# Kernel tuning notes

Hardware: AMD Instinct MI355X
Metric: run time of the kernel (lower is better)

Reference implementation:

```python
import jax, jax.numpy as jnp
import numpy as np

B, T = 64, 16            # batch, action horizon
ACTION_DIM = 32
HIDDEN = 1536            # config.input_embedding_dim
NUM_CAT = 4              # config.max_num_embodiments
NUM_BUCKETS = 1000       # config.num_timestep_buckets


def setup_inputs() -> dict:
    key = jax.random.key(0)
    ks = jax.random.split(key, 6)
    return {
        "actions": jax.random.normal(ks[0], (B, T, ACTION_DIM), jnp.float32),
        "timesteps": jax.random.randint(ks[1], (B,), 0, NUM_BUCKETS, dtype=jnp.int32),
        "cat_ids": jax.random.randint(ks[2], (B,), 0, NUM_CAT, dtype=jnp.int32),
        # CategorySpecificLinear params: W ~ 0.02*randn, b = zeros (as in torch init)
        "W1": 0.02 * jax.random.normal(ks[3], (NUM_CAT, ACTION_DIM, HIDDEN), jnp.float32),
        "b1": jnp.zeros((NUM_CAT, HIDDEN), jnp.float32),
        "W2": 0.02 * jax.random.normal(ks[4], (NUM_CAT, 2 * HIDDEN, HIDDEN), jnp.float32),
        "b2": jnp.zeros((NUM_CAT, HIDDEN), jnp.float32),
        "W3": 0.02 * jax.random.normal(ks[5], (NUM_CAT, HIDDEN, HIDDEN), jnp.float32),
        "b3": jnp.zeros((NUM_CAT, HIDDEN), jnp.float32),
    }


def cs_linear(x, W, b, onehot):
    """CategorySpecificLinear: equivalent to bmm(x, W[cat_ids]) + b[cat_ids].
    Grouped form avoids materializing the (B, Din, Dout) gathered weight tensor:
    compute per-category results (C=4 is tiny) and select via one-hot.
    x: (B,T,Din)  W: (C,Din,Dout)  b: (C,Dout)  onehot: (B,C)
    """
    y = jnp.einsum('btd,cdh->bcth', x, W)        # (B,C,T,Dout)
    y = jnp.einsum('bcth,bc->bth', y, onehot)    # select own category
    return y + (onehot @ b)[:, None, :]


def sinusoidal_pe(t, dim):
    """Standard sinusoidal positional encoding of scalar positions t (B,T) -> (B,T,dim)."""
    half = dim // 2
    freqs = jnp.exp(-np.log(10000.0) * jnp.arange(half, dtype=jnp.float32) / half)
    ang = t.astype(jnp.float32)[..., None] * freqs  # (B,T,half)
    return jnp.concatenate([jnp.sin(ang), jnp.cos(ang)], axis=-1)


def reference(actions, timesteps, cat_ids, W1, b1, W2, b2, W3, b3):
    onehot = jax.nn.one_hot(cat_ids, W1.shape[0], dtype=actions.dtype)  # (B,C)
    t = jnp.broadcast_to(timesteps[:, None], actions.shape[:2])          # (B,T)
    a_emb = cs_linear(actions, W1, b1, onehot)                            # (B,T,H)
    tau_emb = sinusoidal_pe(t, a_emb.shape[-1]).astype(a_emb.dtype)       # (B,T,H)
    x = jnp.concatenate([a_emb, tau_emb], axis=-1)                        # (B,T,2H)
    h = cs_linear(x, W2, b2, onehot)
    h = h * jax.nn.sigmoid(h)                                             # swish
    return cs_linear(h, W3, b3, onehot)                                   # (B,T,H)
```

## Files before the change

### kernel.cpp

```cpp
#include <hip/hip_runtime.h>
#include <hip/hip_bf16.h>

#define BB 64
#define TT 16
#define ROWS 1024
#define ADIM 32
#define HID 1536
#define NCAT 4
#define MT_MAX 20

typedef __attribute__((ext_vector_type(8))) short bf16x8;
typedef __attribute__((ext_vector_type(4))) float f32x4;

static __device__ __forceinline__ unsigned short f2bf(float f) {
    union { float f; unsigned int u; } v; v.f = f;
    unsigned int u = v.u + 0x7fff + ((v.u >> 16) & 1);
    return (unsigned short)(u >> 16);
}

__global__ void prep_kernel(const int* __restrict__ cat_ids,
                            int* __restrict__ msample, int* __restrict__ mcat) {
    __shared__ int counts[NCAT];
    const int t = threadIdx.x;
    if (t < NCAT) {
        int c = 0;
        for (int s = 0; s < BB; ++s) c += (cat_ids[s] == t);
        counts[t] = c;
    }
    __syncthreads();
    if (t < NCAT) {
        int off = 0;
        for (int c = 0; c < t; ++c) off += (counts[c] + 3) >> 2;
        const int mt = (counts[t] + 3) >> 2;
        int idx = 0;
        for (int s = 0; s < BB; ++s)
            if (cat_ids[s] == t) msample[off * 4 + (idx++)] = s;
        for (; idx < mt * 4; ++idx) msample[off * 4 + idx] = -1;
        for (int m = 0; m < mt; ++m) mcat[off + m] = t;
    }
    __syncthreads();
    if (t == 0) {
        int tot = 0;
        for (int c = 0; c < NCAT; ++c) tot += (counts[c] + 3) >> 2;
        for (int m = tot; m < MT_MAX; ++m) mcat[m] = -1;
    }
}

__global__ void build_x_kernel(const float* __restrict__ actions,
                               const int* __restrict__ timesteps,
                               const int* __restrict__ cat_ids,
                               const float* __restrict__ W1,
                               const float* __restrict__ b1,
                               unsigned short* __restrict__ X) {
    const int s = blockIdx.x;
    const int part = blockIdx.y;
    const int t = threadIdx.x;
    if (part < 6) {
        const int cat = cat_ids[s];
        const int h = part * 256 + t;
        __shared__ float act[TT][ADIM];
        const float* ab = actions + (size_t)s * TT * ADIM;
        ((float*)act)[t]       = ab[t];
        ((float*)act)[t + 256] = ab[t + 256];
        __syncthreads();
        const float* W1c = W1 + (size_t)cat * ADIM * HID + h;
        float acc[TT];
        #pragma unroll
        for (int r = 0; r < TT; ++r) acc[r] = 0.f;
        #pragma unroll 8
        for (int d = 0; d < ADIM; ++d) {
            const float w = W1c[(size_t)d * HID];
            #pragma unroll
            for (int r = 0; r < TT; ++r) acc[r] += act[r][d] * w;
        }
        const float bias = b1[cat * HID + h];
        #pragma unroll
        for (int r = 0; r < TT; ++r)
            X[(size_t)(s * TT + r) * (2 * HID) + h] = f2bf(acc[r] + bias);
    } else {
        const float ts = (float)timesteps[s];
        #pragma unroll
        for (int j = 0; j < 6; ++j) {
            const int i = j * 256 + t;
            const int ii = (i < 768) ? i : i - 768;
            const float freq = expf(-9.210340371976184f * (float)ii * (1.0f / 768.0f));
            const float ang = ts * freq;
            const float v = (i < 768) ? sinf(ang) : cosf(ang);
            const unsigned short bv = f2bf(v);
            for (int r = 0; r < TT; ++r)
                X[(size_t)(s * TT + r) * (2 * HID) + HID + i] = bv;
        }
    }
}

template<int K, int S>
__global__ __launch_bounds__(64) void gemm_part_kernel(
        const unsigned short* __restrict__ X,
        const float* __restrict__ W,
        const int* __restrict__ msample,
        const int* __restrict__ mcat,
        float* __restrict__ P) {
    const int m = blockIdx.y;
    const int cat = mcat[m];
    if (cat < 0) return;
    const int n0 = blockIdx.x * 64;
    const int ks = blockIdx.z;
    constexpr int KP = K / S;
    const int k0 = ks * KP;
    const int lane = threadIdx.x;
    const int col = lane & 15;
    const int g = lane >> 4;

    int sidx[4];
    #pragma unroll
    for (int f = 0; f < 4; ++f) sidx[f] = msample[m * 4 + f];

    const unsigned short* arow[4];
    #pragma unroll
    for (int f = 0; f < 4; ++f) {
        const int s = sidx[f] < 0 ? 0 : sidx[f];
        arow[f] = X + (size_t)(s * TT + col) * K + k0 + g * 8;
    }
    const float* wbase = W + ((size_t)cat * K + k0 + g * 8) * HID + n0 + col;

    f32x4 acc[4][4];
    #pragma unroll
    for (int f = 0; f < 4; ++f)
        #pragma unroll
        for (int c = 0; c < 4; ++c) acc[f][c] = f32x4{0.f, 0.f, 0.f, 0.f};

    for (int kk = 0; kk < KP; kk += 32) {
        bf16x8 a[4];
        #pragma unroll
        for (int f = 0; f < 4; ++f)
            a[f] = *(const bf16x8*)(arow[f] + kk);
        const float* wp = wbase + (size_t)kk * HID;
        #pragma unroll
        for (int c = 0; c < 4; ++c) {
            bf16x8 b;
            #pragma unroll
            for (int j = 0; j < 8; ++j) {
                const float w = wp[(size_t)j * HID + c * 16];
                b[j] = (short)f2bf(w);
            }
            #pragma unroll
            for (int f = 0; f < 4; ++f)
                acc[f][c] = __builtin_amdgcn_mfma_f32_16x16x32_bf16(a[f], b, acc[f][c], 0, 0, 0);
        }
    }

    #pragma unroll
    for (int f = 0; f < 4; ++f) {
        if (sidx[f] < 0) continue;
        #pragma unroll
        for (int c = 0; c < 4; ++c) {
            #pragma unroll
            for (int r = 0; r < 4; ++r) {
                const int row = sidx[f] * TT + g * 4 + r;
                P[((size_t)ks * ROWS + row) * HID + n0 + c * 16 + col] = acc[f][c][r];
            }
        }
    }
}

template<int S, bool DOSWISH, bool BF16OUT>
__global__ void finish_kernel(const float* __restrict__ P,
                              const float* __restrict__ bias,
                              const int* __restrict__ cat_ids,
                              void* __restrict__ out) {
    const int idx = blockIdx.x * 256 + threadIdx.x;
    const int i4 = idx * 4;
    const int row = i4 / HID;
    const int colb = i4 - row * HID;
    const int cat = cat_ids[row >> 4];
    float4 v = *(const float4*)(P + i4);
    #pragma unroll
    for (int s2 = 1; s2 < S; ++s2) {
        const float4 p = *(const float4*)(P + (size_t)s2 * ROWS * HID + i4);
        v.x += p.x; v.y += p.y; v.z += p.z; v.w += p.w;
    }
    const float4 bv = *(const float4*)(bias + (size_t)cat * HID + colb);
    v.x += bv.x; v.y += bv.y; v.z += bv.z; v.w += bv.w;
    if (DOSWISH) {
        v.x = v.x / (1.f + __expf(-v.x));
        v.y = v.y / (1.f + __expf(-v.y));
        v.z = v.z / (1.f + __expf(-v.z));
        v.w = v.w / (1.f + __expf(-v.w));
    }
    if (BF16OUT) {
        uint2 u;
        u.x = (unsigned)f2bf(v.x) | ((unsigned)f2bf(v.y) << 16);
        u.y = (unsigned)f2bf(v.z) | ((unsigned)f2bf(v.w) << 16);
        *(uint2*)((unsigned short*)out + i4) = u;
    } else {
        *(float4*)((float*)out + i4) = v;
    }
}

extern "C" void kernel_launch(void* const* d_in, const int* in_sizes, int n_in,
                              void* d_out, int out_size, void* d_ws, size_t ws_size,
                              hipStream_t stream) {
    const float* actions   = (const float*)d_in[0];
    const int*   timesteps = (const int*)d_in[1];
    const int*   cat_ids   = (const int*)d_in[2];
    const float* W1        = (const float*)d_in[3];
    const float* b1        = (const float*)d_in[4];
    const float* W2        = (const float*)d_in[5];
    const float* b2        = (const float*)d_in[6];
    const float* W3        = (const float*)d_in[7];
    const float* b3        = (const float*)d_in[8];

    char* ws = (char*)d_ws;
    unsigned short* X = (unsigned short*)ws;
    unsigned short* H = (unsigned short*)(ws + 6291456);
    float* P          = (float*)(ws + 9437184);
    int* msample      = (int*)(ws + 34603008);
    int* mcat         = msample + MT_MAX * 4;

    prep_kernel<<<1, 64, 0, stream>>>(cat_ids, msample, mcat);
    build_x_kernel<<<dim3(BB, 7), 256, 0, stream>>>(actions, timesteps, cat_ids, W1, b1, X);

    gemm_part_kernel<2 * HID, 4><<<dim3(HID / 64, MT_MAX, 4), 64, 0, stream>>>(
        X, W2, msample, mcat, P);
    finish_kernel<4, true, true><<<ROWS * HID / 4 / 256, 256, 0, stream>>>(
        P, b2, cat_ids, H);

    gemm_part_kernel<HID, 4><<<dim3(HID / 64, MT_MAX, 4), 64, 0, stream>>>(
        H, W3, msample, mcat, P);
    finish_kernel<4, false, false><<<ROWS * HID / 4 / 256, 256, 0, stream>>>(
        P, b3, cat_ids, d_out);
}
```

Baseline: 102.8 us.

## Rewrite grouped GEMM with LDS double-buffered 64x128 tiles and fewer K splits

After: 123.9 us. 20.4% more time.

```diff
diff --git a/kernel.cpp b/kernel.cpp
--- a/kernel.cpp
+++ b/kernel.cpp
@@ -1,5 +1,6 @@
 #include <hip/hip_runtime.h>
 #include <hip/hip_bf16.h>
+#include <stdint.h>
 
 #define BB 64
 #define TT 16
@@ -8,6 +9,8 @@
 #define HID 1536
 #define NCAT 4
 #define MT_MAX 20
+#define KP 768
+#define NTILES (KP/64)
 
 typedef __attribute__((ext_vector_type(8))) short bf16x8;
 typedef __attribute__((ext_vector_type(4))) float f32x4;
@@ -36,13 +39,13 @@
         for (int s = 0; s < BB; ++s)
             if (cat_ids[s] == t) msample[off * 4 + (idx++)] = s;
         for (; idx < mt * 4; ++idx) msample[off * 4 + idx] = -1;
-        for (int m = 0; m < mt; ++m) mcat[off + m] = t;
+        for (int mm = 0; mm < mt; ++mm) mcat[off + mm] = t;
     }
     __syncthreads();
     if (t == 0) {
         int tot = 0;
         for (int c = 0; c < NCAT; ++c) tot += (counts[c] + 3) >> 2;
-        for (int m = tot; m < MT_MAX; ++m) mcat[m] = -1;
+        for (int mm = tot; mm < MT_MAX; ++mm) mcat[mm] = -1;
     }
 }
 
@@ -69,9 +72,9 @@
         for (int r = 0; r < TT; ++r) acc[r] = 0.f;
         #pragma unroll 8
         for (int d = 0; d < ADIM; ++d) {
-            const float w = W1c[(size_t)d * HID];
-            #pragma unroll
-            for (int r = 0; r < TT; ++r) acc[r] += act[r][d] * w;
+            const float wv = W1c[(size_t)d * HID];
+            #pragma unroll
+            for (int r = 0; r < TT; ++r) acc[r] += act[r][d] * wv;
         }
         const float bias = b1[cat * HID + h];
         #pragma unroll
@@ -93,73 +96,135 @@
     }
 }
 
-template<int K, int S>
-__global__ __launch_bounds__(64) void gemm_part_kernel(
-        const unsigned short* __restrict__ X,
+template<int K>
+__global__ __launch_bounds__(256) void gemm_cs2(
+        const unsigned short* __restrict__ Xin,
         const float* __restrict__ W,
         const int* __restrict__ msample,
         const int* __restrict__ mcat,
         float* __restrict__ P) {
-    const int m = blockIdx.y;
+    const int m   = blockIdx.y;
     const int cat = mcat[m];
     if (cat < 0) return;
-    const int n0 = blockIdx.x * 64;
+    const int n0 = blockIdx.x * 128;
     const int ks = blockIdx.z;
-    constexpr int KP = K / S;
     const int k0 = ks * KP;
-    const int lane = threadIdx.x;
-    const int col = lane & 15;
-    const int g = lane >> 4;
-
-    int sidx[4];
+
+    const int q  = threadIdx.x;
+    const int l  = q & 63;
+    const int w  = q >> 6;
+    const int wm = w >> 1, wn = w & 1;
+    const int col = l & 15, g = l >> 4;
+
+    __shared__ unsigned short Abuf[2][8][64][8];
+    __shared__ unsigned short Bbuf[2][8][128][8];
+
+    const int s0 = msample[m*4+0], s1 = msample[m*4+1],
+              s2 = msample[m*4+2], s3 = msample[m*4+3];
+
+    int sA = (g == 0) ? s0 : (g == 1) ? s1 : (g == 2) ? s2 : s3;
+    if (sA < 0) sA = 0;
+    const unsigned short* aSrc = Xin + ((size_t)sA * TT + col) * K + k0;
+
+    const float* wbase = W + ((size_t)cat * K + k0) * HID + n0;
+
+    f32x4 acc[2][4];
     #pragma unroll
-    for (int f = 0; f < 4; ++f) sidx[f] = msample[m * 4 + f];
-
-    const unsigned short* arow[4];
+    for (int i = 0; i < 2; ++i)
+        #pragma unroll
+        for (int j = 0; j < 4; ++j) acc[i][j] = f32x4{0.f, 0.f, 0.f, 0.f};
+
+    float bcol[4][8];
+
+#if __has_builtin(__builtin_amdgcn_global_load_lds)
+    auto issueA = [&](int t, int buf) {
+        #pragma unroll
+        for (int pp = 0; pp < 2; ++pp) {
+            const int p = w * 2 + pp;
+            __builtin_amdgcn_global_load_lds(
+                (const __attribute__((address_space(1))) unsigned int*)(aSrc + t * 64 + p * 8),
+                (__attribute__((address_space(3))) unsigned int*)(&Abuf[buf][p][0][0]),
+                16, 0, 0);
+        }
+    };
+#else
+    const int rowF = q >> 2;
+    int sF = (w == 0) ? s0 : (w == 1) ? s1 : (w == 2) ? s2 : s3;
+    if (sF < 0) sF = 0;
+    const unsigned short* aSrcF = Xin + ((size_t)sF * TT + (rowF & 15)) * K + k0;
+    auto issueA = [&](int t, int buf) {
+        #pragma unroll
+        for (int it = 0; it < 2; ++it) {
+            const int slot = (q & 3) + it * 4;
+            bf16x8 av = *(const bf16x8*)(aSrcF + t * 64 + slot * 8);
+            *(bf16x8*)(&Abuf[buf][slot][rowF][0]) = av;
+        }
+    };
+#endif
+
+    auto loadB = [&](int t) {
+        #pragma unroll
+        for (int it = 0; it < 4; ++it) {
+            const int c = q + it * 256;
+            const int n = c & 127, slot = c >> 7;
+            const float* wc = wbase + ((size_t)t * 64 + slot * 8) * HID + n;
+            #pragma unroll
+            for (int dk = 0; dk < 8; ++dk) bcol[it][dk] = wc[(size_t)dk * HID];
+        }
+    };
+    auto cvtWriteB = [&](int buf) {
+        #pragma unroll
+        for (int it = 0; it < 4; ++it) {
+            const int c = q + it * 256;
+            const int n = c & 127, slot = c >> 7;
+            bf16x8 v;
+            #pragma unroll
+            for (int dk = 0; dk < 8; ++dk) v[dk] = (short)f2bf(bcol[it][dk]);
+            *(bf16x8*)(&Bbuf[buf][slot][n][0]) = v;
+        }
+    };
+    auto compute = [&](int buf) {
+        #pragma unroll
+        for (int kc = 0; kc < 2; ++kc) {
+            const int sl = kc * 4 + g;
+            const bf16x8 a0 = *(const bf16x8*)(&Abuf[buf][sl][wm * 32 + col][0]);
+            const bf16x8 a1 = *(const bf16x8*)(&Abuf[buf][sl][wm * 32 + 16 + col][0]);
+            #pragma unroll
+            for (int nf = 0; nf < 4; ++nf) {
+                const bf16x8 bb = *(const bf16x8*)(&Bbuf[buf][sl][wn * 64 + nf * 16 + col][0]);
+                acc[0][nf] = __builtin_amdgcn_mfma_f32_16x16x32_bf16(a0, bb, acc[0][nf], 0, 0, 0);
+                acc[1][nf] = __builtin_amdgcn_mfma_f32_16x16x32_bf16(a1, bb, acc[1][nf], 0, 0, 0);
+            }
+        }
+    };
+
+    issueA(0, 0);
+    loadB(0);
+    cvtWriteB(0);
+    __syncthreads();
+    for (int t = 0; t < NTILES - 1; ++t) {
+        const int cur = t & 1, nxt = cur ^ 1;
+        loadB(t + 1);
+        issueA(t + 1, nxt);
+        compute(cur);
+        cvtWriteB(nxt);
+        __syncthreads();
+    }
+    compute((NTILES - 1) & 1);
+
+    const int sE0 = wm ? s2 : s0;
+    const int sE1 = wm ? s3 : s1;
     #pragma unroll
-    for (int f = 0; f < 4; ++f) {
-        const int s = sidx[f] < 0 ? 0 : sidx[f];
-        arow[f] = X + (size_t)(s * TT + col) * K + k0 + g * 8;
-    }
-    const float* wbase = W + ((size_t)cat * K + k0 + g * 8) * HID + n0 + col;
-
-    f32x4 acc[4][4];
-    #pragma unroll
-    for (int f = 0; f < 4; ++f)
-        #pragma unroll
-        for (int c = 0; c < 4; ++c) acc[f][c] = f32x4{0.f, 0.f, 0.f, 0.f};
-
-    for (int kk = 0; kk < KP; kk += 32) {
-        bf16x8 a[4];
-        #pragma unroll
-        for (int f = 0; f < 4; ++f)
-            a[f] = *(const bf16x8*)(arow[f] + kk);
-        const float* wp = wbase + (size_t)kk * HID;
-        #pragma unroll
-        for (int c = 0; c < 4; ++c) {
-            bf16x8 b;
-            #pragma unroll
-            for (int j = 0; j < 8; ++j) {
-                const float w = wp[(size_t)j * HID + c * 16];
-                b[j] = (short)f2bf(w);
-            }
-            #pragma unroll
-            for (int f = 0; f < 4; ++f)
-                acc[f][c] = __builtin_amdgcn_mfma_f32_16x16x32_bf16(a[f], b, acc[f][c], 0, 0, 0);
-        }
-    }
-
-    #pragma unroll
-    for (int f = 0; f < 4; ++f) {
-        if (sidx[f] < 0) continue;
-        #pragma unroll
-        for (int c = 0; c < 4; ++c) {
-            #pragma unroll
-            for (int r = 0; r < 4; ++r) {
-                const int row = sidx[f] * TT + g * 4 + r;
-                P[((size_t)ks * ROWS + row) * HID + n0 + c * 16 + col] = acc[f][c][r];
-            }
-        }
+    for (int mf = 0; mf < 2; ++mf) {
+        const int s = mf ? sE1 : sE0;
+        if (s < 0) continue;
+        float* prow = P + ((size_t)ks * ROWS + (size_t)s * TT + g * 4) * HID
+                        + n0 + wn * 64 + col;
+        #pragma unroll
+        for (int nf = 0; nf < 4; ++nf)
+            #pragma unroll
+            for (int j = 0; j < 4; ++j)
+                prow[(size_t)j * HID + nf * 16] = acc[mf][nf][j];
     }
 }
 
@@ -220,13 +285,13 @@
     prep_kernel<<<1, 64, 0, stream>>>(cat_ids, msample, mcat);
     build_x_kernel<<<dim3(BB, 7), 256, 0, stream>>>(actions, timesteps, cat_ids, W1, b1, X);
 
-    gemm_part_kernel<2 * HID, 4><<<dim3(HID / 64, MT_MAX, 4), 64, 0, stream>>>(
+    gemm_cs2<2 * HID><<<dim3(HID / 128, MT_MAX, 4), 256, 0, stream>>>(
         X, W2, msample, mcat, P);
     finish_kernel<4, true, true><<<ROWS * HID / 4 / 256, 256, 0, stream>>>(
         P, b2, cat_ids, H);
 
-    gemm_part_kernel<HID, 4><<<dim3(HID / 64, MT_MAX, 4), 64, 0, stream>>>(
+    gemm_cs2<HID><<<dim3(HID / 128, MT_MAX, 2), 256, 0, stream>>>(
         H, W3, msample, mcat, P);
-    finish_kernel<4, false, false><<<ROWS * HID / 4 / 256, 256, 0, stream>>>(
+    finish_kernel<2, false, false><<<ROWS * HID / 4 / 256, 256, 0, stream>>>(
         P, b3, cat_ids, d_out);
 }
```

## Software-pipeline GEMM loads with triple-buffered registers and reduce W3 split-K

Applied to the files above, without the earlier changes.

Measured after the change: 119.6 us. +16.3%, slower.

```diff
diff --git a/kernel.cpp b/kernel.cpp
--- a/kernel.cpp
+++ b/kernel.cpp
@@ -36,13 +36,13 @@
         for (int s = 0; s < BB; ++s)
             if (cat_ids[s] == t) msample[off * 4 + (idx++)] = s;
         for (; idx < mt * 4; ++idx) msample[off * 4 + idx] = -1;
-        for (int m = 0; m < mt; ++m) mcat[off + m] = t;
+        for (int mm = 0; mm < mt; ++mm) mcat[off + mm] = t;
     }
     __syncthreads();
     if (t == 0) {
         int tot = 0;
         for (int c = 0; c < NCAT; ++c) tot += (counts[c] + 3) >> 2;
-        for (int m = tot; m < MT_MAX; ++m) mcat[m] = -1;
+        for (int mm = tot; mm < MT_MAX; ++mm) mcat[mm] = -1;
     }
 }
 
@@ -69,9 +69,9 @@
         for (int r = 0; r < TT; ++r) acc[r] = 0.f;
         #pragma unroll 8
         for (int d = 0; d < ADIM; ++d) {
-            const float w = W1c[(size_t)d * HID];
-            #pragma unroll
-            for (int r = 0; r < TT; ++r) acc[r] += act[r][d] * w;
+            const float wv = W1c[(size_t)d * HID];
+            #pragma unroll
+            for (int r = 0; r < TT; ++r) acc[r] += act[r][d] * wv;
         }
         const float bias = b1[cat * HID + h];
         #pragma unroll
@@ -93,73 +93,100 @@
     }
 }
 
-template<int K, int S>
-__global__ __launch_bounds__(64) void gemm_part_kernel(
-        const unsigned short* __restrict__ X,
+template<int K, int KSPLIT>
+__global__ __launch_bounds__(64, 2) void gemm_sw(
+        const unsigned short* __restrict__ Xin,
         const float* __restrict__ W,
         const int* __restrict__ msample,
         const int* __restrict__ mcat,
         float* __restrict__ P) {
-    const int m = blockIdx.y;
+    constexpr int KP = K / KSPLIT;
+    constexpr int NT = KP / 32;
+    static_assert(NT % 3 == 0, "NT must be divisible by 3");
+
+    const int m   = blockIdx.y;
     const int cat = mcat[m];
     if (cat < 0) return;
     const int n0 = blockIdx.x * 64;
     const int ks = blockIdx.z;
-    constexpr int KP = K / S;
     const int k0 = ks * KP;
-    const int lane = threadIdx.x;
-    const int col = lane & 15;
-    const int g = lane >> 4;
+
+    const int l   = threadIdx.x;
+    const int col = l & 15;
+    const int g   = l >> 4;
 
     int sidx[4];
     #pragma unroll
     for (int f = 0; f < 4; ++f) sidx[f] = msample[m * 4 + f];
 
-    const unsigned short* arow[4];
+    const unsigned short* aptr[4];
     #pragma unroll
     for (int f = 0; f < 4; ++f) {
         const int s = sidx[f] < 0 ? 0 : sidx[f];
-        arow[f] = X + (size_t)(s * TT + col) * K + k0 + g * 8;
-    }
-    const float* wbase = W + ((size_t)cat * K + k0 + g * 8) * HID + n0 + col;
+        aptr[f] = Xin + ((size_t)s * TT + col) * K + k0 + g * 8;
+    }
+    const float* wptr = W + ((size_t)cat * K + k0 + g * 8) * HID + n0 + col;
 
     f32x4 acc[4][4];
     #pragma unroll
-    for (int f = 0; f < 4; ++f)
-        #pragma unroll
-        for (int c = 0; c < 4; ++c) acc[f][c] = f32x4{0.f, 0.f, 0.f, 0.f};
-
-    for (int kk = 0; kk < KP; kk += 32) {
-        bf16x8 a[4];
+    for (int i = 0; i < 4; ++i)
+        #pragma unroll
+        for (int j = 0; j < 4; ++j) acc[i][j] = f32x4{0.f, 0.f, 0.f, 0.f};
+
+    float  bs[3][32];
+    bf16x8 as[3][4];
+
+    auto issueB = [&](int t, int s) {
+        const int tc = (t < NT) ? t : NT - 1;
+        #pragma unroll
+        for (int nf = 0; nf < 4; ++nf)
+            #pragma unroll
+            for (int j = 0; j < 8; ++j)
+                bs[s][nf * 8 + j] = wptr[(size_t)(tc * 32 + j) * HID + nf * 16];
+    };
+    auto issueA = [&](int t, int s) {
+        const int tc = (t < NT) ? t : NT - 1;
         #pragma unroll
         for (int f = 0; f < 4; ++f)
-            a[f] = *(const bf16x8*)(arow[f] + kk);
-        const float* wp = wbase + (size_t)kk * HID;
-        #pragma unroll
-        for (int c = 0; c < 4; ++c) {
-            bf16x8 b;
-            #pragma unroll
-            for (int j = 0; j < 8; ++j) {
-                const float w = wp[(size_t)j * HID + c * 16];
-                b[j] = (short)f2bf(w);
-            }
-            #pragma unroll
-            for (int f = 0; f < 4; ++f)
-                acc[f][c] = __builtin_amdgcn_mfma_f32_16x16x32_bf16(a[f], b, acc[f][c], 0, 0, 0);
-        }
-    }
-
-    #pragma unroll
-    for (int f = 0; f < 4; ++f) {
-        if (sidx[f] < 0) continue;
-        #pragma unroll
-        for (int c = 0; c < 4; ++c) {
-            #pragma unroll
-            for (int r = 0; r < 4; ++r) {
-                const int row = sidx[f] * TT + g * 4 + r;
-                P[((size_t)ks * ROWS + row) * HID + n0 + c * 16 + col] = acc[f][c][r];
-            }
-        }
+            as[s][f] = *(const bf16x8*)(aptr[f] + tc * 32);
+    };
+    auto step = [&](int s) {
+        bf16x8 bfr[4];
+        #pragma unroll
+        for (int nf = 0; nf < 4; ++nf)
+            #pragma unroll
+            for (int j = 0; j < 8; ++j)
+                bfr[nf][j] = (short)f2bf(bs[s][nf * 8 + j]);
+        #pragma unroll
+        for (int mf = 0; mf < 4; ++mf)
+            #pragma unroll
+            for (int nf = 0; nf < 4; ++nf)
+                acc[mf][nf] = __builtin_amdgcn_mfma_f32_16x16x32_bf16(
+                    as[s][mf], bfr[nf], acc[mf][nf], 0, 0, 0);
+    };
+
+    issueB(0, 0); issueA(0, 0);
+    issueB(1, 1); issueA(1, 1);
+
+    for (int tt = 0; tt < NT; tt += 3) {
+        issueB(tt + 2, 2); issueA(tt + 2, 2);
+        step(0);
+        issueB(tt + 3, 0); issueA(tt + 3, 0);
+        step(1);
+        issueB(tt + 4, 1); issueA(tt + 4, 1);
+        step(2);
+    }
+
+    #pragma unroll
+    for (int mf = 0; mf < 4; ++mf) {
+        if (sidx[mf] < 0) continue;
+        float* prow = P + ((size_t)ks * ROWS + (size_t)sidx[mf] * TT + g * 4) * HID
+                        + n0 + col;
+        #pragma unroll
+        for (int nf = 0; nf < 4; ++nf)
+            #pragma unroll
+            for (int r = 0; r < 4; ++r)
+                prow[(size_t)r * HID + nf * 16] = acc[mf][nf][r];
     }
 }
 
@@ -220,13 +247,13 @@
     prep_kernel<<<1, 64, 0, stream>>>(cat_ids, msample, mcat);
     build_x_kernel<<<dim3(BB, 7), 256, 0, stream>>>(actions, timesteps, cat_ids, W1, b1, X);
 
-    gemm_part_kernel<2 * HID, 4><<<dim3(HID / 64, MT_MAX, 4), 64, 0, stream>>>(
+    gemm_sw<2 * HID, 4><<<dim3(HID / 64, MT_MAX, 4), 64, 0, stream>>>(
         X, W2, msample, mcat, P);
     finish_kernel<4, true, true><<<ROWS * HID / 4 / 256, 256, 0, stream>>>(
         P, b2, cat_ids, H);
 
-    gemm_part_kernel<HID, 4><<<dim3(HID / 64, MT_MAX, 4), 64, 0, stream>>>(
+    gemm_sw<HID, 2><<<dim3(HID / 64, MT_MAX, 2), 64, 0, stream>>>(
         H, W3, msample, mcat, P);
-    finish_kernel<4, false, false><<<ROWS * HID / 4 / 256, 256, 0, stream>>>(
+    finish_kernel<2, false, false><<<ROWS * HID / 4 / 256, 256, 0, stream>>>(
         P, b3, cat_ids, d_out);
 }
```
